# Optimization experiments

Hardware: AMD Instinct MI355X
Metric: run time of the kernel (lower is better)

The kernel has to match this reference:

```python
import jax, jax.numpy as jnp
import numpy as np

S, B, T = 512, 256, 128


def setup_inputs() -> dict:
    key = jax.random.key(0)
    k1, k2, k3, k4, k5, k6 = jax.random.split(key, 6)
    emissions = jax.random.normal(k1, (S, B, T), dtype=jnp.float32)
    # realistic monotone mask: each sequence has a random length in [1, S]
    lengths = jax.random.randint(k2, (B,), 1, S + 1)
    mask = (jnp.arange(S)[:, None] < lengths[None, :]).astype(jnp.float32)  # [S,B]
    tags = jax.random.randint(k3, (S, B), 0, T)
    transitions = jax.random.normal(k4, (T, T), dtype=jnp.float32)
    start_transitions = jax.random.normal(k5, (T,), dtype=jnp.float32)
    stop_transitions = jax.random.normal(k6, (T,), dtype=jnp.float32)
    return {
        "emissions": emissions,
        "mask": mask,
        "tags": tags,
        "transitions": transitions,
        "start_transitions": start_transitions,
        "stop_transitions": stop_transitions,
    }


def reference(emissions, mask, tags, transitions, start_transitions, stop_transitions):
    seq_len, batch, num_tags = emissions.shape

    # ---- log-partition (forward algorithm) + viterbi score, fused scan ----
    init = start_transitions + emissions[0]  # [B,T]

    def part_step(carry, xs):
        fv, vv = carry  # forward var, viterbi var: [B,T]
        em, m = xs      # em: [B,T], m: [B]
        # scores[b, j, k] = em[b, j] + transitions[j, k]  (j=next tag, k=prev tag)
        scores = em[:, :, None] + transitions[None, :, :]          # [B,T,T]
        lse = jax.nn.logsumexp(fv[:, None, :] + scores, axis=2)     # [B,T]
        vmax = jnp.max(vv[:, None, :] + scores, axis=2)             # [B,T]
        fv = m[:, None] * lse + (1.0 - m)[:, None] * fv
        vv = m[:, None] * vmax + (1.0 - m)[:, None] * vv
        return (fv, vv), None

    (fv, vv), _ = jax.lax.scan(part_step, (init, init), (emissions[1:], mask[1:]))
    total_score = jax.nn.logsumexp(fv + stop_transitions, axis=1)   # [B]
    best_path_score = jnp.max(vv + stop_transitions, axis=1)        # [B]

    # ---- gold path score ----
    barange = jnp.arange(batch)
    tag0 = tags[0]
    rps0 = start_transitions[tag0] + emissions[0, barange, tag0] * mask[0]

    def rp_step(carry, xs):
        rps, prev = carry
        cur, em, m = xs  # cur:[B] int, em:[B,T], m:[B]
        rps = rps + transitions[prev, cur] * m
        rps = rps + jnp.take_along_axis(em, cur[:, None], axis=1)[:, 0] * m
        prev = jnp.where(m == 1.0, cur, prev)
        return (rps, prev), None

    (rps, prev), _ = jax.lax.scan(rp_step, (rps0, tag0), (tags[1:], emissions[1:], mask[1:]))
    real_path_score = rps + stop_transitions[prev]

    loss = jnp.mean(total_score - real_path_score)
    return loss, real_path_score, total_score, best_path_score
```

## Files before the change

### kernel.cpp

```cpp
#include <hip/hip_runtime.h>
#include <math.h>

#define S_LEN 512
#define BATCH 256
#define NTAG  128
#define EMSTRIDE (BATCH * NTAG)

typedef float f32x4 __attribute__((ext_vector_type(4)));
typedef float f32x2 __attribute__((ext_vector_type(2)));

__device__ __forceinline__ int lidx(int k) { return k + ((k >> 6) << 2); }
__device__ __forceinline__ f32x2 lo2(f32x4 v){ f32x2 r; r[0]=v[0]; r[1]=v[1]; return r; }
__device__ __forceinline__ f32x2 hi2(f32x4 v){ f32x2 r; r[0]=v[2]; r[1]=v[3]; return r; }
__device__ __forceinline__ f32x2 pmax2(f32x2 a, f32x2 b){
  f32x2 r; r[0]=fmaxf(a[0],b[0]); r[1]=fmaxf(a[1],b[1]); return r;
}

#define DPP_XOR1(x) __int_as_float(__builtin_amdgcn_mov_dpp(__float_as_int(x), 0xB1, 0xF, 0xF, false))

#define BAR() do {                                       \
    asm volatile("s_waitcnt lgkmcnt(0)" ::: "memory");   \
    __builtin_amdgcn_s_barrier();                        \
    __builtin_amdgcn_sched_barrier(0);                   \
  } while (0)

__global__ __launch_bounds__(256, 1)
void crf_fat_kernel(const float* __restrict__ emis,
                    const float* __restrict__ mask,
                    const int* __restrict__ tags,
                    const float* __restrict__ trans,
                    const float* __restrict__ startt,
                    const float* __restrict__ stopt,
                    float* __restrict__ ws,
                    int* __restrict__ ewbuf,
                    float* __restrict__ out)
{
  const int blk  = blockIdx.x;
  const int tid  = threadIdx.x;
  const int role = blk >> 8;
  const int b    = blk & 255;
  const int lane = tid & 63;
  const int wid  = tid >> 6;

  __shared__ __align__(16) float sbuf[2][144];
  __shared__ float red[8];

  if (role == 4) {
    float part = 0.f, lenp = 0.f;
#pragma unroll
    for (int rep = 0; rep < 2; ++rep) {
      int s = tid + rep * 256;
      float m  = mask[(size_t)s * BATCH + b];
      int  cur = tags[(size_t)s * BATCH + b];
      if (s == 0) {
        part += startt[cur] + emis[(size_t)b * NTAG + cur] * m;
      } else {
        int prev = tags[(size_t)(s - 1) * BATCH + b];
        part += m * (trans[(size_t)prev * NTAG + cur] +
                     emis[((size_t)s * BATCH + b) * NTAG + cur]);
      }
      lenp += m;
    }
#pragma unroll
    for (int d = 1; d <= 32; d <<= 1) {
      part += __shfl_xor(part, d);
      lenp += __shfl_xor(lenp, d);
    }
    if (lane == 0) { red[wid] = part; red[4 + wid] = lenp; }
    __syncthreads();
    if (tid == 0) {
      float rps = (red[0] + red[1]) + (red[2] + red[3]);
      float lf  = (red[4] + red[5]) + (red[6] + red[7]);
      int len = (int)(lf + 0.5f);
      int pf  = tags[(size_t)(len - 1) * BATCH + b];
      out[1 + b] = rps + stopt[pf];
    }
    return;
  }

  const int p    = tid >> 1;
  const int h    = tid & 1;
  const int widx = lidx(p);

  int len;
  {
    float mv = mask[(size_t)tid * BATCH + b] +
               mask[(size_t)(tid + 256) * BATCH + b];
#pragma unroll
    for (int d = 1; d <= 32; d <<= 1) mv += __shfl_xor(mv, d);
    if (lane == 0) red[wid] = mv;
    __syncthreads();
    float ls = (red[0] + red[1]) + (red[2] + red[3]);
    len = (int)(ls + 0.5f);
    len = __builtin_amdgcn_readfirstlane(len);
  }
  const int sm     = (len - 1) >> 1;
  const int nsteps = len - 1 - sm;
  const float* eb  = emis + (size_t)b * NTAG + p;

  if (role == 0) {
    f32x2 E2[32];
    {
      const float* tr = trans + (size_t)p * NTAG + 64 * h;
#pragma unroll
      for (int c = 0; c < 16; ++c) {
        f32x4 t = *(const f32x4*)(tr + 4 * c);
        f32x2 a, bb;
        a[0] = __expf(t[0]); a[1] = __expf(t[1]);
        bb[0] = __expf(t[2]); bb[1] = __expf(t[3]);
        E2[2*c] = a; E2[2*c+1] = bb;
      }
    }
    if (h == 0) sbuf[0][widx] = __expf(startt[p] + eb[0]);
    float e0 = eb[(size_t)1 * EMSTRIDE];
    float e1 = eb[(size_t)2 * EMSTRIDE];
    float e2 = eb[(size_t)3 * EMSTRIDE];
    float e3 = eb[(size_t)4 * EMSTRIDE];
    int Ew = 0, fin = 0;
    __syncthreads();

#define FSTEP(U, EXV, RENORM)                                                 \
  {                                                                           \
    if (g + (U) > sm) { fin = (U) & 1; goto epi_f; }                          \
    const f32x4* wr = (const f32x4*)(sbuf[(U) & 1] + 68 * h);                 \
    f32x2 a0 = {0.f, 0.f}, a1 = {0.f, 0.f}, r2 = {0.f, 0.f};                  \
    _Pragma("unroll")                                                         \
    for (int c = 0; c < 16; ++c) {                                            \
      f32x4 w = wr[c];                                                        \
      f32x2 wl = lo2(w), wh = hi2(w);                                         \
      a0 = a0 + E2[2*c] * wl;                                                 \
      a1 = a1 + E2[2*c+1] * wh;                                               \
      if (RENORM) r2 = pmax2(r2, pmax2(wl, wh));                              \
    }                                                                         \
    f32x2 as = a0 + a1;                                                       \
    float sum = as[0] + as[1];                                                \
    sum += DPP_XOR1(sum);                                                     \
    float uf;                                                                 \
    if (RENORM) {                                                             \
      float rw = fmaxf(r2[0], r2[1]);                                         \
      rw = fmaxf(rw, DPP_XOR1(rw));                                           \
      int ew = (int)((__float_as_uint(rw) >> 23) & 0xFF) - 126;               \
      Ew += ew;                                                               \
      float swc = __uint_as_float((unsigned)(127 - ew) << 23);                \
      uf = (EXV) * sum * swc;                                                 \
    } else {                                                                  \
      uf = (EXV) * sum;                                                       \
    }                                                                         \
    if (h == 0) sbuf[((U) + 1) & 1][widx] = uf;                               \
    BAR();                                                                    \
  }

    for (int g = 1; g < S_LEN; g += 4) {
      int c0 = g + 4 < S_LEN ? g + 4 : S_LEN - 1;
      int c1 = g + 5 < S_LEN ? g + 5 : S_LEN - 1;
      int c2 = g + 6 < S_LEN ? g + 6 : S_LEN - 1;
      int c3 = g + 7 < S_LEN ? g + 7 : S_LEN - 1;
      float n0 = eb[(size_t)c0 * EMSTRIDE];
      float n1 = eb[(size_t)c1 * EMSTRIDE];
      float n2 = eb[(size_t)c2 * EMSTRIDE];
      float n3 = eb[(size_t)c3 * EMSTRIDE];
      float x0 = __expf(e0), x1 = __expf(e1);
      float x2 = __expf(e2), x3 = __expf(e3);
      FSTEP(0, x0, 0)
      FSTEP(1, x1, 0)
      FSTEP(2, x2, 0)
      FSTEP(3, x3, 1)
      e0 = n0; e1 = n1; e2 = n2; e3 = n3;
    }
    fin = 0;
epi_f:
    {
      if (tid < 128) ws[(size_t)b * 512 + tid] = sbuf[fin][lidx(tid)];
      if (tid == 0) ewbuf[b] = Ew;
    }
  } else if (role == 1) {
    f32x2 E2[32];
    {
      const float* tc = trans + p + (size_t)(64 * h) * NTAG;
#pragma unroll
      for (int e = 0; e < 32; ++e) {
        f32x2 a;
        a[0] = __expf(tc[(size_t)(2*e)     * NTAG]);
        a[1] = __expf(tc[(size_t)(2*e + 1) * NTAG]);
        E2[e] = a;
      }
    }
    if (h == 0) {
      float st = stopt[p];
      float y = (nsteps > 0) ? __expf(st + eb[(size_t)(len - 1) * EMSTRIDE])
                             : __expf(st);
      sbuf[0][widx] = y;
    }
    int s0i = len - 2;     s0i = s0i < 0 ? 0 : s0i;
    int s1i = len - 3;     s1i = s1i < 0 ? 0 : s1i;
    int s2i = len - 4;     s2i = s2i < 0 ? 0 : s2i;
    int s3i = len - 5;     s3i = s3i < 0 ? 0 : s3i;
    float e0 = eb[(size_t)s0i * EMSTRIDE];
    float e1 = eb[(size_t)s1i * EMSTRIDE];
    float e2 = eb[(size_t)s2i * EMSTRIDE];
    float e3 = eb[(size_t)s3i * EMSTRIDE];
    int Ew = 0, fin = 0;
    __syncthreads();

#define BSTEP(U, EXV, RENORM)                                                 \
  {                                                                           \
    if (gi + (U) >= nsteps) { fin = (U) & 1; goto epi_b; }                    \
    const f32x4* wr = (const f32x4*)(sbuf[(U) & 1] + 68 * h);                 \
    f32x2 a0 = {0.f, 0.f}, a1 = {0.f, 0.f}, r2 = {0.f, 0.f};                  \
    _Pragma("unroll")                                                         \
    for (int c = 0; c < 16; ++c) {                                            \
      f32x4 w = wr[c];                                                        \
      f32x2 wl = lo2(w), wh = hi2(w);                                         \
      a0 = a0 + E2[2*c] * wl;                                                 \
      a1 = a1 + E2[2*c+1] * wh;                                               \
      if (RENORM) r2 = pmax2(r2, pmax2(wl, wh));                              \
    }                                                                         \
    f32x2 as = a0 + a1;                                                       \
    float sum = as[0] + as[1];                                                \
    sum += DPP_XOR1(sum);                                                     \
    float exm = (gi + (U) == nsteps - 1) ? 1.0f : (EXV);                      \
    float uf;                                                                 \
    if (RENORM) {                                                             \
      float rw = fmaxf(r2[0], r2[1]);                                         \
      rw = fmaxf(rw, DPP_XOR1(rw));                                           \
      int ew = (int)((__float_as_uint(rw) >> 23) & 0xFF) - 126;               \
      Ew += ew;                                                               \
      float swc = __uint_as_float((unsigned)(127 - ew) << 23);                \
      uf = exm * sum * swc;                                                   \
    } else {                                                                  \
      uf = exm * sum;                                                         \
    }                                                                         \
    if (h == 0) sbuf[((U) + 1) & 1][widx] = uf;                               \
    BAR();                                                                    \
  }

    for (int gi = 0; gi < S_LEN; gi += 4) {
      int c0 = len - 2 - (gi + 4); c0 = c0 < 0 ? 0 : c0;
      int c1 = len - 2 - (gi + 5); c1 = c1 < 0 ? 0 : c1;
      int c2 = len - 2 - (gi + 6); c2 = c2 < 0 ? 0 : c2;
      int c3 = len - 2 - (gi + 7); c3 = c3 < 0 ? 0 : c3;
      float n0 = eb[(size_t)c0 * EMSTRIDE];
      float n1 = eb[(size_t)c1 * EMSTRIDE];
      float n2 = eb[(size_t)c2 * EMSTRIDE];
      float n3 = eb[(size_t)c3 * EMSTRIDE];
      float x0 = __expf(e0), x1 = __expf(e1);
      float x2 = __expf(e2), x3 = __expf(e3);
      BSTEP(0, x0, 0)
      BSTEP(1, x1, 0)
      BSTEP(2, x2, 0)
      BSTEP(3, x3, 1)
      e0 = n0; e1 = n1; e2 = n2; e3 = n3;
    }
    fin = 0;
epi_b:
    {
      if (tid < 128) ws[(size_t)b * 512 + 128 + tid] = sbuf[fin][lidx(tid)];
      if (tid == 0) ewbuf[BATCH + b] = Ew;
    }
  } else if (role == 2) {
    f32x2 T2[32];
    {
      const float* tr = trans + (size_t)p * NTAG + 64 * h;
#pragma unroll
      for (int c = 0; c < 16; ++c) {
        f32x4 t = *(const f32x4*)(tr + 4 * c);
        T2[2*c]   = lo2(t);
        T2[2*c+1] = hi2(t);
      }
    }
    if (h == 0) sbuf[0][widx] = startt[p] + eb[0];
    float e0 = eb[(size_t)1 * EMSTRIDE];
    float e1 = eb[(size_t)2 * EMSTRIDE];
    float e2 = eb[(size_t)3 * EMSTRIDE];
    float e3 = eb[(size_t)4 * EMSTRIDE];
    int fin = 0;
    __syncthreads();

#define VSTEP(U, EMV)                                                         \
  {                                                                           \
    if (g + (U) > sm) { fin = (U) & 1; goto epi_v; }                          \
    const f32x4* vr = (const f32x4*)(sbuf[(U) & 1] + 68 * h);                 \
    f32x2 m2 = {-3.0e38f, -3.0e38f};                                          \
    _Pragma("unroll")                                                         \
    for (int c = 0; c < 16; ++c) {                                            \
      f32x4 v = vr[c];                                                        \
      m2 = pmax2(m2, pmax2(lo2(v) + T2[2*c], hi2(v) + T2[2*c+1]));            \
    }                                                                         \
    float vm = fmaxf(m2[0], m2[1]);                                           \
    vm = fmaxf(vm, DPP_XOR1(vm));                                             \
    float uv = (EMV) + vm;                                                    \
    if (h == 0) sbuf[((U) + 1) & 1][widx] = uv;                               \
    BAR();                                                                    \
  }

    for (int g = 1; g < S_LEN; g += 4) {
      int c0 = g + 4 < S_LEN ? g + 4 : S_LEN - 1;
      int c1 = g + 5 < S_LEN ? g + 5 : S_LEN - 1;
      int c2 = g + 6 < S_LEN ? g + 6 : S_LEN - 1;
      int c3 = g + 7 < S_LEN ? g + 7 : S_LEN - 1;
      float n0 = eb[(size_t)c0 * EMSTRIDE];
      float n1 = eb[(size_t)c1 * EMSTRIDE];
      float n2 = eb[(size_t)c2 * EMSTRIDE];
      float n3 = eb[(size_t)c3 * EMSTRIDE];
      VSTEP(0, e0)
      VSTEP(1, e1)
      VSTEP(2, e2)
      VSTEP(3, e3)
      e0 = n0; e1 = n1; e2 = n2; e3 = n3;
    }
    fin = 0;
epi_v:
    {
      if (tid < 128) ws[(size_t)b * 512 + 256 + tid] = sbuf[fin][lidx(tid)];
    }
  } else {
    f32x2 T2[32];
    {
      const float* tc = trans + p + (size_t)(64 * h) * NTAG;
#pragma unroll
      for (int e = 0; e < 32; ++e) {
        f32x2 a;
        a[0] = tc[(size_t)(2*e)     * NTAG];
        a[1] = tc[(size_t)(2*e + 1) * NTAG];
        T2[e] = a;
      }
    }
    if (h == 0) {
      float st = stopt[p];
      float y = (nsteps > 0) ? st + eb[(size_t)(len - 1) * EMSTRIDE] : st;
      sbuf[0][widx] = y;
    }
    int s0i = len - 2;     s0i = s0i < 0 ? 0 : s0i;
    int s1i = len - 3;     s1i = s1i < 0 ? 0 : s1i;
    int s2i = len - 4;     s2i = s2i < 0 ? 0 : s2i;
    int s3i = len - 5;     s3i = s3i < 0 ? 0 : s3i;
    float e0 = eb[(size_t)s0i * EMSTRIDE];
    float e1 = eb[(size_t)s1i * EMSTRIDE];
    float e2 = eb[(size_t)s2i * EMSTRIDE];
    float e3 = eb[(size_t)s3i * EMSTRIDE];
    int fin = 0;
    __syncthreads();

#define WSTEP(U, EMV)                                                         \
  {                                                                           \
    if (gi + (U) >= nsteps) { fin = (U) & 1; goto epi_w; }                    \
    const f32x4* vr = (const f32x4*)(sbuf[(U) & 1] + 68 * h);                 \
    f32x2 m2 = {-3.0e38f, -3.0e38f};                                          \
    _Pragma("unroll")                                                         \
    for (int c = 0; c < 16; ++c) {                                            \
      f32x4 v = vr[c];                                                        \
      m2 = pmax2(m2, pmax2(lo2(v) + T2[2*c], hi2(v) + T2[2*c+1]));            \
    }                                                                         \
    float vm = fmaxf(m2[0], m2[1]);                                           \
    vm = fmaxf(vm, DPP_XOR1(vm));                                             \
    float uv = (gi + (U) == nsteps - 1) ? vm : vm + (EMV);                    \
    if (h == 0) sbuf[((U) + 1) & 1][widx] = uv;                               \
    BAR();                                                                    \
  }

    for (int gi = 0; gi < S_LEN; gi += 4) {
      int c0 = len - 2 - (gi + 4); c0 = c0 < 0 ? 0 : c0;
      int c1 = len - 2 - (gi + 5); c1 = c1 < 0 ? 0 : c1;
      int c2 = len - 2 - (gi + 6); c2 = c2 < 0 ? 0 : c2;
      int c3 = len - 2 - (gi + 7); c3 = c3 < 0 ? 0 : c3;
      float n0 = eb[(size_t)c0 * EMSTRIDE];
      float n1 = eb[(size_t)c1 * EMSTRIDE];
      float n2 = eb[(size_t)c2 * EMSTRIDE];
      float n3 = eb[(size_t)c3 * EMSTRIDE];
      WSTEP(0, e0)
      WSTEP(1, e1)
      WSTEP(2, e2)
      WSTEP(3, e3)
      e0 = n0; e1 = n1; e2 = n2; e3 = n3;
    }
    fin = 0;
epi_w:
    {
      if (tid < 128) ws[(size_t)b * 512 + 384 + tid] = sbuf[fin][lidx(tid)];
    }
  }
}

__global__ __launch_bounds__(128, 1)
void crf_combine_kernel(const float* __restrict__ ws,
                        const int* __restrict__ ewbuf,
                        float* __restrict__ out)
{
  const int b = blockIdx.x, k = threadIdx.x;
  const float* base = ws + (size_t)b * 512;
  float t1 = base[k] * base[128 + k];
  float m1 = base[256 + k] + base[384 + k];
#pragma unroll
  for (int d = 1; d <= 32; d <<= 1) {
    t1 += __shfl_xor(t1, d);
    m1 = fmaxf(m1, __shfl_xor(m1, d));
  }
  __shared__ float rs[2], rm[2];
  const int lane = k & 63, wid = k >> 6;
  if (lane == 0) { rs[wid] = t1; rm[wid] = m1; }
  __syncthreads();
  if (k == 0) {
    const double LN2 = 0.6931471805599453;
    int Et = ewbuf[b] + ewbuf[BATCH + b];
    out[1 + BATCH + b]     = (float)((double)Et * LN2 + (double)__logf(rs[0] + rs[1]));
    out[1 + 2 * BATCH + b] = fmaxf(rm[0], rm[1]);
  }
}

__global__ __launch_bounds__(256, 1)
void crf_loss_kernel(float* __restrict__ out)
{
  const int tid = threadIdx.x;
  float dft = out[1 + BATCH + tid] - out[1 + tid];
#pragma unroll
  for (int d = 1; d <= 32; d <<= 1) dft += __shfl_xor(dft, d);
  __shared__ float rs[4];
  const int lane = tid & 63, wid = tid >> 6;
  if (lane == 0) rs[wid] = dft;
  __syncthreads();
  if (tid == 0)
    out[0] = ((rs[0] + rs[1]) + (rs[2] + rs[3])) * (1.0f / BATCH);
}

extern "C" void kernel_launch(void* const* d_in, const int* in_sizes, int n_in,
                              void* d_out, int out_size, void* d_ws, size_t ws_size,
                              hipStream_t stream)
{
  const float* emis   = (const float*)d_in[0];
  const float* mask   = (const float*)d_in[1];
  const int*   tags   = (const int*)d_in[2];
  const float* trans  = (const float*)d_in[3];
  const float* startt = (const float*)d_in[4];
  const float* stopt  = (const float*)d_in[5];
  float* out = (float*)d_out;

  float* wsf   = (float*)d_ws;
  int*   ewbuf = (int*)(wsf + 512 * BATCH);

  crf_fat_kernel<<<5 * BATCH, 256, 0, stream>>>(emis, mask, tags, trans,
                                                startt, stopt, wsf, ewbuf, out);
  crf_combine_kernel<<<BATCH, 128, 0, stream>>>(wsf, ewbuf, out);
  crf_loss_kernel<<<1, 256, 0, stream>>>(out);
}
```

Before: 210.0 us.

## Split each tag's reduction across four threads with 512-thread blocks

Each tag row is now reduced by four threads instead of two, so the fat kernel launches with 512 threads per block. Each thread handles a 32-element slice, and partials are combined with two DPP xor steps. The shared-memory layout uses a new swizzle, accumulation uses explicit FMAs and max3, and the emission exp moves inside each step. This shortens the serial per-step dependency chain of the sequential scan. In exchange, every per-step barrier now has to synchronise eight waves instead of four, and the mask reduction runs over 512 threads.

```diff
diff --git a/kernel.cpp b/kernel.cpp
--- a/kernel.cpp
+++ b/kernel.cpp
@@ -9,14 +9,16 @@
 typedef float f32x4 __attribute__((ext_vector_type(4)));
 typedef float f32x2 __attribute__((ext_vector_type(2)));
 
-__device__ __forceinline__ int lidx(int k) { return k + ((k >> 6) << 2); }
+__device__ __forceinline__ int swz(int k) { return k + ((k >> 5) << 3); }
+
 __device__ __forceinline__ f32x2 lo2(f32x4 v){ f32x2 r; r[0]=v[0]; r[1]=v[1]; return r; }
 __device__ __forceinline__ f32x2 hi2(f32x4 v){ f32x2 r; r[0]=v[2]; r[1]=v[3]; return r; }
-__device__ __forceinline__ f32x2 pmax2(f32x2 a, f32x2 b){
-  f32x2 r; r[0]=fmaxf(a[0],b[0]); r[1]=fmaxf(a[1],b[1]); return r;
-}
+__device__ __forceinline__ f32x2 pmax2(f32x2 a, f32x2 b){ f32x2 r; r[0]=fmaxf(a[0],b[0]); r[1]=fmaxf(a[1],b[1]); return r; }
+__device__ __forceinline__ f32x2 fma2(f32x2 a, f32x2 b, f32x2 c){ f32x2 r; r[0]=__builtin_fmaf(a[0],b[0],c[0]); r[1]=__builtin_fmaf(a[1],b[1],c[1]); return r; }
+__device__ __forceinline__ float max3f(float a, float b, float c){ return fmaxf(fmaxf(a,b),c); }
 
 #define DPP_XOR1(x) __int_as_float(__builtin_amdgcn_mov_dpp(__float_as_int(x), 0xB1, 0xF, 0xF, false))
+#define DPP_XOR2(x) __int_as_float(__builtin_amdgcn_mov_dpp(__float_as_int(x), 0x4E, 0xF, 0xF, false))
 
 #define BAR() do {                                       \
     asm volatile("s_waitcnt lgkmcnt(0)" ::: "memory");   \
@@ -24,7 +26,7 @@
     __builtin_amdgcn_sched_barrier(0);                   \
   } while (0)
 
-__global__ __launch_bounds__(256, 1)
+__global__ __launch_bounds__(512, 1)
 void crf_fat_kernel(const float* __restrict__ emis,
                     const float* __restrict__ mask,
                     const int* __restrict__ tags,
@@ -42,35 +44,32 @@
   const int lane = tid & 63;
   const int wid  = tid >> 6;
 
-  __shared__ __align__(16) float sbuf[2][144];
-  __shared__ float red[8];
+  __shared__ __align__(16) float sbuf[2][160];
+  __shared__ float red[16];
 
   if (role == 4) {
-    float part = 0.f, lenp = 0.f;
-#pragma unroll
-    for (int rep = 0; rep < 2; ++rep) {
-      int s = tid + rep * 256;
-      float m  = mask[(size_t)s * BATCH + b];
-      int  cur = tags[(size_t)s * BATCH + b];
-      if (s == 0) {
-        part += startt[cur] + emis[(size_t)b * NTAG + cur] * m;
-      } else {
-        int prev = tags[(size_t)(s - 1) * BATCH + b];
-        part += m * (trans[(size_t)prev * NTAG + cur] +
-                     emis[((size_t)s * BATCH + b) * NTAG + cur]);
-      }
-      lenp += m;
+    const int s = tid;
+    float m  = mask[(size_t)s * BATCH + b];
+    int  cur = tags[(size_t)s * BATCH + b];
+    float part, lenp = m;
+    if (s == 0) {
+      part = startt[cur] + emis[(size_t)b * NTAG + cur] * m;
+    } else {
+      int prev = tags[(size_t)(s - 1) * BATCH + b];
+      part = m * (trans[(size_t)prev * NTAG + cur] +
+                  emis[((size_t)s * BATCH + b) * NTAG + cur]);
     }
 #pragma unroll
     for (int d = 1; d <= 32; d <<= 1) {
       part += __shfl_xor(part, d);
       lenp += __shfl_xor(lenp, d);
     }
-    if (lane == 0) { red[wid] = part; red[4 + wid] = lenp; }
+    if (lane == 0) { red[wid] = part; red[8 + wid] = lenp; }
     __syncthreads();
     if (tid == 0) {
-      float rps = (red[0] + red[1]) + (red[2] + red[3]);
-      float lf  = (red[4] + red[5]) + (red[6] + red[7]);
+      float rps = 0.f, lf = 0.f;
+#pragma unroll
+      for (int w = 0; w < 8; ++w) { rps += red[w]; lf += red[8 + w]; }
       int len = (int)(lf + 0.5f);
       int pf  = tags[(size_t)(len - 1) * BATCH + b];
       out[1 + b] = rps + stopt[pf];
@@ -78,40 +77,41 @@
     return;
   }
 
-  const int p    = tid >> 1;
-  const int h    = tid & 1;
-  const int widx = lidx(p);
+  const int h   = tid & 3;
+  const int j   = tid >> 2;
+  const int base = 10 * h;
 
   int len;
   {
-    float mv = mask[(size_t)tid * BATCH + b] +
-               mask[(size_t)(tid + 256) * BATCH + b];
+    float mv = mask[(size_t)tid * BATCH + b];
 #pragma unroll
     for (int d = 1; d <= 32; d <<= 1) mv += __shfl_xor(mv, d);
     if (lane == 0) red[wid] = mv;
     __syncthreads();
-    float ls = (red[0] + red[1]) + (red[2] + red[3]);
+    float ls = 0.f;
+#pragma unroll
+    for (int w = 0; w < 8; ++w) ls += red[w];
     len = (int)(ls + 0.5f);
     len = __builtin_amdgcn_readfirstlane(len);
   }
   const int sm     = (len - 1) >> 1;
   const int nsteps = len - 1 - sm;
-  const float* eb  = emis + (size_t)b * NTAG + p;
+  const float* eb  = emis + (size_t)b * NTAG + j;
 
   if (role == 0) {
-    f32x2 E2[32];
+    f32x2 E2[16];
     {
-      const float* tr = trans + (size_t)p * NTAG + 64 * h;
-#pragma unroll
-      for (int c = 0; c < 16; ++c) {
+      const float* tr = trans + (size_t)j * NTAG + 32 * h;
+#pragma unroll
+      for (int c = 0; c < 8; ++c) {
         f32x4 t = *(const f32x4*)(tr + 4 * c);
         f32x2 a, bb;
-        a[0] = __expf(t[0]); a[1] = __expf(t[1]);
+        a[0] = __expf(t[0]);  a[1] = __expf(t[1]);
         bb[0] = __expf(t[2]); bb[1] = __expf(t[3]);
         E2[2*c] = a; E2[2*c+1] = bb;
       }
     }
-    if (h == 0) sbuf[0][widx] = __expf(startt[p] + eb[0]);
+    if (h == 0) sbuf[0][swz(j)] = __expf(startt[j] + eb[0]);
     float e0 = eb[(size_t)1 * EMSTRIDE];
     float e1 = eb[(size_t)2 * EMSTRIDE];
     float e2 = eb[(size_t)3 * EMSTRIDE];
@@ -119,34 +119,35 @@
     int Ew = 0, fin = 0;
     __syncthreads();
 
-#define FSTEP(U, EXV, RENORM)                                                 \
+#define FSTEP(U, EMV, RENORM)                                                 \
   {                                                                           \
     if (g + (U) > sm) { fin = (U) & 1; goto epi_f; }                          \
-    const f32x4* wr = (const f32x4*)(sbuf[(U) & 1] + 68 * h);                 \
-    f32x2 a0 = {0.f, 0.f}, a1 = {0.f, 0.f}, r2 = {0.f, 0.f};                  \
+    const f32x4* wr = (const f32x4*)sbuf[(U) & 1];                            \
+    f32x2 a0 = {0.f,0.f}, a1 = {0.f,0.f}, r2 = {0.f,0.f};                     \
     _Pragma("unroll")                                                         \
-    for (int c = 0; c < 16; ++c) {                                            \
-      f32x4 w = wr[c];                                                        \
+    for (int c = 0; c < 8; ++c) {                                             \
+      f32x4 w = wr[base + c];                                                 \
       f32x2 wl = lo2(w), wh = hi2(w);                                         \
-      a0 = a0 + E2[2*c] * wl;                                                 \
-      a1 = a1 + E2[2*c+1] * wh;                                               \
+      a0 = fma2(E2[2*c],   wl, a0);                                           \
+      a1 = fma2(E2[2*c+1], wh, a1);                                           \
       if (RENORM) r2 = pmax2(r2, pmax2(wl, wh));                              \
     }                                                                         \
     f32x2 as = a0 + a1;                                                       \
     float sum = as[0] + as[1];                                                \
-    sum += DPP_XOR1(sum);                                                     \
+    sum += DPP_XOR1(sum); sum += DPP_XOR2(sum);                               \
+    float ex = __expf(EMV);                                                   \
     float uf;                                                                 \
     if (RENORM) {                                                             \
       float rw = fmaxf(r2[0], r2[1]);                                         \
-      rw = fmaxf(rw, DPP_XOR1(rw));                                           \
+      rw = fmaxf(rw, DPP_XOR1(rw)); rw = fmaxf(rw, DPP_XOR2(rw));             \
       int ew = (int)((__float_as_uint(rw) >> 23) & 0xFF) - 126;               \
       Ew += ew;                                                               \
       float swc = __uint_as_float((unsigned)(127 - ew) << 23);                \
-      uf = (EXV) * sum * swc;                                                 \
+      uf = ex * sum * swc;                                                    \
     } else {                                                                  \
-      uf = (EXV) * sum;                                                       \
-    }                                                                         \
-    if (h == 0) sbuf[((U) + 1) & 1][widx] = uf;                               \
+      uf = ex * sum;                                                          \
+    }                                                                         \
+    if (h == 0) sbuf[((U) + 1) & 1][swz(j)] = uf;                             \
     BAR();                                                                    \
   }
 
@@ -159,42 +160,37 @@
       float n1 = eb[(size_t)c1 * EMSTRIDE];
       float n2 = eb[(size_t)c2 * EMSTRIDE];
       float n3 = eb[(size_t)c3 * EMSTRIDE];
-      float x0 = __expf(e0), x1 = __expf(e1);
-      float x2 = __expf(e2), x3 = __expf(e3);
-      FSTEP(0, x0, 0)
-      FSTEP(1, x1, 0)
-      FSTEP(2, x2, 0)
-      FSTEP(3, x3, 1)
+      FSTEP(0, e0, 0)
+      FSTEP(1, e1, 0)
+      FSTEP(2, e2, 0)
+      FSTEP(3, e3, 1)
       e0 = n0; e1 = n1; e2 = n2; e3 = n3;
     }
     fin = 0;
 epi_f:
+    if (tid < 128) ws[(size_t)b * 512 + tid] = sbuf[fin][swz(tid)];
+    if (tid == 0) ewbuf[b] = Ew;
+  } else if (role == 1) {
+    f32x2 E2[16];
     {
-      if (tid < 128) ws[(size_t)b * 512 + tid] = sbuf[fin][lidx(tid)];
-      if (tid == 0) ewbuf[b] = Ew;
-    }
-  } else if (role == 1) {
-    f32x2 E2[32];
-    {
-      const float* tc = trans + p + (size_t)(64 * h) * NTAG;
-#pragma unroll
-      for (int e = 0; e < 32; ++e) {
+      const float* tc = trans + j + (size_t)(32 * h) * NTAG;
+#pragma unroll
+      for (int q = 0; q < 16; ++q) {
         f32x2 a;
-        a[0] = __expf(tc[(size_t)(2*e)     * NTAG]);
-        a[1] = __expf(tc[(size_t)(2*e + 1) * NTAG]);
-        E2[e] = a;
+        a[0] = __expf(tc[(size_t)(2*q)     * NTAG]);
+        a[1] = __expf(tc[(size_t)(2*q + 1) * NTAG]);
+        E2[q] = a;
       }
     }
     if (h == 0) {
-      float st = stopt[p];
-      float y = (nsteps > 0) ? __expf(st + eb[(size_t)(len - 1) * EMSTRIDE])
-                             : __expf(st);
-      sbuf[0][widx] = y;
-    }
-    int s0i = len - 2;     s0i = s0i < 0 ? 0 : s0i;
-    int s1i = len - 3;     s1i = s1i < 0 ? 0 : s1i;
-    int s2i = len - 4;     s2i = s2i < 0 ? 0 : s2i;
-    int s3i = len - 5;     s3i = s3i < 0 ? 0 : s3i;
+      float st = stopt[j];
+      sbuf[0][swz(j)] = (nsteps > 0) ? __expf(st + eb[(size_t)(len - 1) * EMSTRIDE])
+                                     : __expf(st);
+    }
+    int s0i = len - 2; s0i = s0i < 0 ? 0 : s0i;
+    int s1i = len - 3; s1i = s1i < 0 ? 0 : s1i;
+    int s2i = len - 4; s2i = s2i < 0 ? 0 : s2i;
+    int s3i = len - 5; s3i = s3i < 0 ? 0 : s3i;
     float e0 = eb[(size_t)s0i * EMSTRIDE];
     float e1 = eb[(size_t)s1i * EMSTRIDE];
     float e2 = eb[(size_t)s2i * EMSTRIDE];
@@ -202,27 +198,28 @@
     int Ew = 0, fin = 0;
     __syncthreads();
 
-#define BSTEP(U, EXV, RENORM)                                                 \
+#define BSTEP(U, EMV, RENORM)                                                 \
   {                                                                           \
     if (gi + (U) >= nsteps) { fin = (U) & 1; goto epi_b; }                    \
-    const f32x4* wr = (const f32x4*)(sbuf[(U) & 1] + 68 * h);                 \
-    f32x2 a0 = {0.f, 0.f}, a1 = {0.f, 0.f}, r2 = {0.f, 0.f};                  \
+    const f32x4* wr = (const f32x4*)sbuf[(U) & 1];                            \
+    f32x2 a0 = {0.f,0.f}, a1 = {0.f,0.f}, r2 = {0.f,0.f};                     \
     _Pragma("unroll")                                                         \
-    for (int c = 0; c < 16; ++c) {                                            \
-      f32x4 w = wr[c];                                                        \
+    for (int c = 0; c < 8; ++c) {                                             \
+      f32x4 w = wr[base + c];                                                 \
       f32x2 wl = lo2(w), wh = hi2(w);                                         \
-      a0 = a0 + E2[2*c] * wl;                                                 \
-      a1 = a1 + E2[2*c+1] * wh;                                               \
+      a0 = fma2(E2[2*c],   wl, a0);                                           \
+      a1 = fma2(E2[2*c+1], wh, a1);                                           \
       if (RENORM) r2 = pmax2(r2, pmax2(wl, wh));                              \
     }                                                                         \
     f32x2 as = a0 + a1;                                                       \
     float sum = as[0] + as[1];                                                \
-    sum += DPP_XOR1(sum);                                                     \
-    float exm = (gi + (U) == nsteps - 1) ? 1.0f : (EXV);                      \
+    sum += DPP_XOR1(sum); sum += DPP_XOR2(sum);                               \
+    float ex  = __expf(EMV);                                                  \
+    float exm = (gi + (U) == nsteps - 1) ? 1.0f : ex;                         \
     float uf;                                                                 \
     if (RENORM) {                                                             \
       float rw = fmaxf(r2[0], r2[1]);                                         \
-      rw = fmaxf(rw, DPP_XOR1(rw));                                           \
+      rw = fmaxf(rw, DPP_XOR1(rw)); rw = fmaxf(rw, DPP_XOR2(rw));             \
       int ew = (int)((__float_as_uint(rw) >> 23) & 0xFF) - 126;               \
       Ew += ew;                                                               \
       float swc = __uint_as_float((unsigned)(127 - ew) << 23);                \
@@ -230,7 +227,7 @@
     } else {                                                                  \
       uf = exm * sum;                                                         \
     }                                                                         \
-    if (h == 0) sbuf[((U) + 1) & 1][widx] = uf;                               \
+    if (h == 0) sbuf[((U) + 1) & 1][swz(j)] = uf;                             \
     BAR();                                                                    \
   }
 
@@ -243,32 +240,28 @@
       float n1 = eb[(size_t)c1 * EMSTRIDE];
       float n2 = eb[(size_t)c2 * EMSTRIDE];
       float n3 = eb[(size_t)c3 * EMSTRIDE];
-      float x0 = __expf(e0), x1 = __expf(e1);
-      float x2 = __expf(e2), x3 = __expf(e3);
-      BSTEP(0, x0, 0)
-      BSTEP(1, x1, 0)
-      BSTEP(2, x2, 0)
-      BSTEP(3, x3, 1)
+      BSTEP(0, e0, 0)
+      BSTEP(1, e1, 0)
+      BSTEP(2, e2, 0)
+      BSTEP(3, e3, 1)
       e0 = n0; e1 = n1; e2 = n2; e3 = n3;
     }
     fin = 0;
 epi_b:
+    if (tid < 128) ws[(size_t)b * 512 + 128 + tid] = sbuf[fin][swz(tid)];
+    if (tid == 0) ewbuf[BATCH + b] = Ew;
+  } else if (role == 2) {
+    f32x2 T2[16];
     {
-      if (tid < 128) ws[(size_t)b * 512 + 128 + tid] = sbuf[fin][lidx(tid)];
-      if (tid == 0) ewbuf[BATCH + b] = Ew;
-    }
-  } else if (role == 2) {
-    f32x2 T2[32];
-    {
-      const float* tr = trans + (size_t)p * NTAG + 64 * h;
-#pragma unroll
-      for (int c = 0; c < 16; ++c) {
+      const float* tr = trans + (size_t)j * NTAG + 32 * h;
+#pragma unroll
+      for (int c = 0; c < 8; ++c) {
         f32x4 t = *(const f32x4*)(tr + 4 * c);
         T2[2*c]   = lo2(t);
         T2[2*c+1] = hi2(t);
       }
     }
-    if (h == 0) sbuf[0][widx] = startt[p] + eb[0];
+    if (h == 0) sbuf[0][swz(j)] = startt[j] + eb[0];
     float e0 = eb[(size_t)1 * EMSTRIDE];
     float e1 = eb[(size_t)2 * EMSTRIDE];
     float e2 = eb[(size_t)3 * EMSTRIDE];
@@ -279,17 +272,19 @@
 #define VSTEP(U, EMV)                                                         \
   {                                                                           \
     if (g + (U) > sm) { fin = (U) & 1; goto epi_v; }                          \
-    const f32x4* vr = (const f32x4*)(sbuf[(U) & 1] + 68 * h);                 \
-    f32x2 m2 = {-3.0e38f, -3.0e38f};                                          \
+    const f32x4* vr = (const f32x4*)sbuf[(U) & 1];                            \
+    float mA = -3.0e38f, mB = -3.0e38f;                                       \
     _Pragma("unroll")                                                         \
-    for (int c = 0; c < 16; ++c) {                                            \
-      f32x4 v = vr[c];                                                        \
-      m2 = pmax2(m2, pmax2(lo2(v) + T2[2*c], hi2(v) + T2[2*c+1]));            \
-    }                                                                         \
-    float vm = fmaxf(m2[0], m2[1]);                                           \
-    vm = fmaxf(vm, DPP_XOR1(vm));                                             \
-    float uv = (EMV) + vm;                                                    \
-    if (h == 0) sbuf[((U) + 1) & 1][widx] = uv;                               \
+    for (int c = 0; c < 8; ++c) {                                             \
+      f32x4 v = vr[base + c];                                                 \
+      f32x2 x0 = lo2(v) + T2[2*c];                                            \
+      f32x2 x1 = hi2(v) + T2[2*c+1];                                          \
+      mA = max3f(mA, x0[0], x0[1]);                                           \
+      mB = max3f(mB, x1[0], x1[1]);                                           \
+    }                                                                         \
+    float vm = fmaxf(mA, mB);                                                 \
+    vm = fmaxf(vm, DPP_XOR1(vm)); vm = fmaxf(vm, DPP_XOR2(vm));               \
+    if (h == 0) sbuf[((U) + 1) & 1][swz(j)] = (EMV) + vm;                     \
     BAR();                                                                    \
   }
 
@@ -310,30 +305,27 @@
     }
     fin = 0;
 epi_v:
+    if (tid < 128) ws[(size_t)b * 512 + 256 + tid] = sbuf[fin][swz(tid)];
+  } else {
+    f32x2 T2[16];
     {
-      if (tid < 128) ws[(size_t)b * 512 + 256 + tid] = sbuf[fin][lidx(tid)];
-    }
-  } else {
-    f32x2 T2[32];
-    {
-      const float* tc = trans + p + (size_t)(64 * h) * NTAG;
-#pragma unroll
-      for (int e = 0; e < 32; ++e) {
+      const float* tc = trans + j + (size_t)(32 * h) * NTAG;
+#pragma unroll
+      for (int q = 0; q < 16; ++q) {
         f32x2 a;
-        a[0] = tc[(size_t)(2*e)     * NTAG];
-        a[1] = tc[(size_t)(2*e + 1) * NTAG];
-        T2[e] = a;
+        a[0] = tc[(size_t)(2*q)     * NTAG];
+        a[1] = tc[(size_t)(2*q + 1) * NTAG];
+        T2[q] = a;
       }
     }
     if (h == 0) {
-      float st = stopt[p];
-      float y = (nsteps > 0) ? st + eb[(size_t)(len - 1) * EMSTRIDE] : st;
-      sbuf[0][widx] = y;
-    }
-    int s0i = len - 2;     s0i = s0i < 0 ? 0 : s0i;
-    int s1i = len - 3;     s1i = s1i < 0 ? 0 : s1i;
-    int s2i = len - 4;     s2i = s2i < 0 ? 0 : s2i;
-    int s3i = len - 5;     s3i = s3i < 0 ? 0 : s3i;
+      float st = stopt[j];
+      sbuf[0][swz(j)] = (nsteps > 0) ? st + eb[(size_t)(len - 1) * EMSTRIDE] : st;
+    }
+    int s0i = len - 2; s0i = s0i < 0 ? 0 : s0i;
+    int s1i = len - 3; s1i = s1i < 0 ? 0 : s1i;
+    int s2i = len - 4; s2i = s2i < 0 ? 0 : s2i;
+    int s3i = len - 5; s3i = s3i < 0 ? 0 : s3i;
     float e0 = eb[(size_t)s0i * EMSTRIDE];
     float e1 = eb[(size_t)s1i * EMSTRIDE];
     float e2 = eb[(size_t)s2i * EMSTRIDE];
@@ -344,17 +336,20 @@
 #define WSTEP(U, EMV)                                                         \
   {                                                                           \
     if (gi + (U) >= nsteps) { fin = (U) & 1; goto epi_w; }                    \
-    const f32x4* vr = (const f32x4*)(sbuf[(U) & 1] + 68 * h);                 \
-    f32x2 m2 = {-3.0e38f, -3.0e38f};                                          \
+    const f32x4* vr = (const f32x4*)sbuf[(U) & 1];                            \
+    float mA = -3.0e38f, mB = -3.0e38f;                                       \
     _Pragma("unroll")                                                         \
-    for (int c = 0; c < 16; ++c) {                                            \
-      f32x4 v = vr[c];                                                        \
-      m2 = pmax2(m2, pmax2(lo2(v) + T2[2*c], hi2(v) + T2[2*c+1]));            \
-    }                                                                         \
-    float vm = fmaxf(m2[0], m2[1]);                                           \
-    vm = fmaxf(vm, DPP_XOR1(vm));                                             \
+    for (int c = 0; c < 8; ++c) {                                             \
+      f32x4 v = vr[base + c];                                                 \
+      f32x2 x0 = lo2(v) + T2[2*c];                                            \
+      f32x2 x1 = hi2(v) + T2[2*c+1];                                          \
+      mA = max3f(mA, x0[0], x0[1]);                                           \
+      mB = max3f(mB, x1[0], x1[1]);                                           \
+    }                                                                         \
+    float vm = fmaxf(mA, mB);                                                 \
+    vm = fmaxf(vm, DPP_XOR1(vm)); vm = fmaxf(vm, DPP_XOR2(vm));               \
     float uv = (gi + (U) == nsteps - 1) ? vm : vm + (EMV);                    \
-    if (h == 0) sbuf[((U) + 1) & 1][widx] = uv;                               \
+    if (h == 0) sbuf[((U) + 1) & 1][swz(j)] = uv;                             \
     BAR();                                                                    \
   }
 
@@ -375,9 +370,7 @@
     }
     fin = 0;
 epi_w:
-    {
-      if (tid < 128) ws[(size_t)b * 512 + 384 + tid] = sbuf[fin][lidx(tid)];
-    }
+    if (tid < 128) ws[(size_t)b * 512 + 384 + tid] = sbuf[fin][swz(tid)];
   }
 }
 
@@ -437,7 +430,7 @@
   float* wsf   = (float*)d_ws;
   int*   ewbuf = (int*)(wsf + 512 * BATCH);
 
-  crf_fat_kernel<<<5 * BATCH, 256, 0, stream>>>(emis, mask, tags, trans,
+  crf_fat_kernel<<<5 * BATCH, 512, 0, stream>>>(emis, mask, tags, trans,
                                                 startt, stopt, wsf, ewbuf, out);
   crf_combine_kernel<<<BATCH, 128, 0, stream>>>(wsf, ewbuf, out);
   crf_loss_kernel<<<1, 256, 0, stream>>>(out);
```

Result: slower. 214.5 us (+2.2%).
